# Kernel optimization log

Hardware: AMD Instinct MI355X
Metric: run time of the kernel (lower is better)

The kernel has to match this reference:

```python
import jax, jax.numpy as jnp
import numpy as np

ATOM_DIM = 34
GAT_DIM = 128
HID_DIM = 256
G_LAYERS = 3
ALPHA = 0.2
NEG_INF = -9e15  # matches torch zero_vec constant


def setup_inputs() -> dict:
    key = jax.random.key(0)
    ks = jax.random.split(key, 10)
    B, N = 64, 512
    compound = jax.random.normal(ks[0], (B, N, ATOM_DIM), dtype=jnp.float32)
    adj = jax.random.randint(ks[1], (B, N, N), 0, 2, dtype=jnp.int32)
    # xavier_uniform gain=1.414 approx: bound = gain*sqrt(6/(fan_in+fan_out))
    def xavier(k, shape, gain=1.414):
        bound = gain * np.sqrt(6.0 / (shape[-2] + shape[-1]))
        return jax.random.uniform(k, shape, jnp.float32, -bound, bound)
    W_stack = xavier(ks[2], (G_LAYERS, ATOM_DIM, GAT_DIM))        # per-layer W
    a_stack = xavier(ks[3], (G_LAYERS, 2 * GAT_DIM, 1))            # per-layer a
    W_out = xavier(ks[4], (G_LAYERS * GAT_DIM, GAT_DIM))           # gat_out.W
    a_out = xavier(ks[5], (2 * GAT_DIM, 1))                        # gat_out.a
    lim = 1.0 / np.sqrt(GAT_DIM)
    Wc = jax.random.uniform(ks[6], (GAT_DIM, HID_DIM), jnp.float32, -lim, lim)  # W_comp weight (in,out)
    bc = jax.random.uniform(ks[7], (HID_DIM,), jnp.float32, -lim, lim)
    return {"compound": compound, "adj": adj, "W_stack": W_stack,
            "a_stack": a_stack, "W_out": W_out, "a_out": a_out,
            "Wc": Wc, "bc": bc}


def _gat_layer(h, adj, W, a, concat):
    # h: [B,N,Fin], adj: [B,N,N], W: [Fin,Fout], a: [2*Fout,1]
    Wh = jnp.einsum('bnf,fg->bng', h, W)                 # [B,N,Fout]
    Fout = W.shape[1]
    # e[b,i,j] = leakyrelu(Wh_i . a1 + Wh_j . a2) == leakyrelu(cat(Wh_i,Wh_j) @ a)
    src = Wh @ a[:Fout, 0]                               # [B,N]
    dst = Wh @ a[Fout:, 0]                               # [B,N]
    e = jax.nn.leaky_relu(src[:, :, None] + dst[:, None, :], ALPHA)  # [B,N,N]
    scores = jnp.where(adj > 0, e, NEG_INF)
    attention = jax.nn.softmax(scores, axis=2)
    h_prime = jnp.einsum('bij,bjf->bif', attention, Wh)  # [B,N,Fout]
    return jax.nn.elu(h_prime) if concat else h_prime


def reference(compound, adj, W_stack, a_stack, W_out, a_out, Wc, bc):
    heads = [_gat_layer(compound, adj, W_stack[l], a_stack[l], concat=True)
             for l in range(G_LAYERS)]
    multi = jnp.concatenate(heads, axis=2)               # [B,N,G_LAYERS*GAT_DIM]
    x = jax.nn.elu(_gat_layer(multi, adj, W_out, a_out, concat=False))
    x = jax.nn.leaky_relu(jnp.einsum('bnf,fh->bnh', x, Wc) + bc, ALPHA)
    return x  # [B,N,HID_DIM]
```

## Files before the change

kernel.cpp:

```cpp
#include <hip/hip_runtime.h>
#include <hip/hip_bf16.h>
#include <math.h>


#define ALPHA 0.2f
#define LOG2E 1.44269504088896f

#if __has_builtin(__builtin_amdgcn_exp2f)
#define EXP2F(x) __builtin_amdgcn_exp2f(x)
#else
extern "C" __device__ float __ocml_exp2_f32(float);
#define EXP2F(x) __ocml_exp2_f32(x)
#endif

typedef __attribute__((ext_vector_type(8))) short s16x8;
typedef __attribute__((ext_vector_type(4))) float f32x4;

#define MF(a, b, c) c = __builtin_amdgcn_mfma_f32_16x16x32_bf16(a, b, c, 0, 0, 0)

__device__ __forceinline__ ushort bf16_rne(float f) {
  union { float f; unsigned u; } v; v.f = f;
  unsigned r = v.u + 0x7FFFu + ((v.u >> 16) & 1u);
  return (ushort)(r >> 16);
}
__device__ __forceinline__ float bf16_tof(ushort h) {
  union { unsigned u; float f; } v; v.u = ((unsigned)h) << 16;
  return v.f;
}
__device__ __forceinline__ void split_store4(
    ushort* __restrict__ ph, ushort* __restrict__ pl,
    float v0, float v1, float v2, float v3) {
  ushort h0 = bf16_rne(v0), h1 = bf16_rne(v1), h2 = bf16_rne(v2), h3 = bf16_rne(v3);
  *(ushort4*)ph = make_ushort4(h0, h1, h2, h3);
  *(ushort4*)pl = make_ushort4(bf16_rne(v0 - bf16_tof(h0)), bf16_rne(v1 - bf16_tof(h1)),
                               bf16_rne(v2 - bf16_tof(h2)), bf16_rne(v3 - bf16_tof(h3)));
}

__device__ __forceinline__ long wht_off(long batch, int c, int j) {
  return batch * 65536 + (long)(c >> 4) * 8192 + (j >> 5) * 512 +
         ((c & 15) << 3) + (((j >> 3) & 3) << 7) + (j & 7);
}

__device__ __forceinline__ long w_frag_off(int c, int j, int Kd) {
  return (long)(c >> 4) * (Kd * 16) + (j >> 5) * 512 +
         ((c & 15) << 3) + (((j >> 3) & 3) << 7) + (j & 7);
}

#define WHT_SLOT 8388608L

__global__ __launch_bounds__(256) void front_union(
    const float* __restrict__ A, const float* __restrict__ Wst,
    const float* __restrict__ ast,
    ushort* __restrict__ whtBase, float* __restrict__ srcB, float* __restrict__ dstB,
    const int* __restrict__ adj, unsigned* __restrict__ mask,
    const float* __restrict__ W_out, ushort* __restrict__ WoT_H, ushort* __restrict__ WoT_L)
{
  __shared__ float AsT[34][36];
  __shared__ float Ws[34][128];
  const int t = threadIdx.x;
  const int g = blockIdx.x / 83, r83 = blockIdx.x - g * 83;

  if (r83 >= 48) {
    if (r83 < 80) {
      const int mb = g * 32 + (r83 - 48);
      const int gid = mb * 256 + t;
      const int4* __restrict__ p = (const int4*)(adj + (long)gid * 32);
      unsigned m = 0;
#pragma unroll
      for (int k = 0; k < 8; k++) {
        const int4 v = p[k];
        m |= (v.x > 0 ? 1u : 0u) << (4 * k);
        m |= (v.y > 0 ? 1u : 0u) << (4 * k + 1);
        m |= (v.z > 0 ? 1u : 0u) << (4 * k + 2);
        m |= (v.w > 0 ? 1u : 0u) << (4 * k + 3);
      }
      mask[gid] = m;
    } else {
      const int wb = g * 3 + (r83 - 80);
      const int idx = wb * 256 + t;
      const int k = idx / 128, n = idx % 128;
      const float v = W_out[idx];
      const ushort h = bf16_rne(v);
      const long o = w_frag_off(n, k, 384);
      WoT_H[o] = h;
      WoT_L[o] = bf16_rne(v - bf16_tof(h));
    }
    return;
  }

  const int bid = g * 48 + r83;
  const int l = bid >> 10;
  const float* __restrict__ W = Wst + (long)l * 34 * 128;
  const float* __restrict__ avec = ast + (long)l * 256;
  ushort* __restrict__ whtH = whtBase + (long)l * WHT_SLOT;
  ushort* __restrict__ whtL = whtH + 4194304;
  float* __restrict__ src = srcB + (long)l * 32768;
  float* __restrict__ dst = dstB + (long)l * 32768;
  const long row0 = (long)(bid & 1023) * 32;
  const int cg = t & 31, rg = t >> 5;
  {
    const int r = t >> 3, l8 = t & 7;
#pragma unroll
    for (int q = 0; q < 5; q++) {
      int k = l8 + q * 8;
      if (k < 34) AsT[k][r] = A[(row0 + r) * 34 + k];
    }
  }
  {
    int idx = t;
#pragma unroll
    for (int i = 0; i < 17; i++, idx += 256)
      Ws[idx >> 7][idx & 127] = W[idx];
  }
  __syncthreads();

  float acc[4][4];
#pragma unroll
  for (int r = 0; r < 4; r++)
#pragma unroll
    for (int c = 0; c < 4; c++) acc[r][c] = 0.f;
#pragma unroll 2
  for (int k = 0; k < 34; k++) {
    const float4 wv = *(const float4*)&Ws[k][cg * 4];
    const float4 av = *(const float4*)&AsT[k][rg * 4];
#define GFMA(r, a) \
    acc[r][0] += (a) * wv.x; acc[r][1] += (a) * wv.y; \
    acc[r][2] += (a) * wv.z; acc[r][3] += (a) * wv.w;
    GFMA(0, av.x) GFMA(1, av.y) GFMA(2, av.z) GFMA(3, av.w)
#undef GFMA
  }

  {
    const long batch = row0 >> 9;
    const int j = (int)(row0 & 511) + rg * 4;
#pragma unroll
    for (int cc = 0; cc < 4; cc++) {
      const long o = wht_off(batch, cg * 4 + cc, j);
      split_store4(&whtH[o], &whtL[o], acc[0][cc], acc[1][cc], acc[2][cc], acc[3][cc]);
    }
  }

  const float4 a1 = *(const float4*)&avec[cg * 4];
  const float4 a2 = *(const float4*)&avec[128 + cg * 4];
#pragma unroll
  for (int r = 0; r < 4; r++) {
    float s = acc[r][0]*a1.x + acc[r][1]*a1.y + acc[r][2]*a1.z + acc[r][3]*a1.w;
    float d = acc[r][0]*a2.x + acc[r][1]*a2.y + acc[r][2]*a2.z + acc[r][3]*a2.w;
#pragma unroll
    for (int w = 1; w < 32; w <<= 1) {
      s += __shfl_xor(s, w, 64);
      d += __shfl_xor(d, w, 64);
    }
    if (cg == 0) {
      src[row0 + rg * 4 + r] = s * LOG2E;
      dst[row0 + rg * 4 + r] = d * LOG2E;
    }
  }
}


#define LD_SET(S, KB) \
  S##0H = *(const s16x8*)&bH[(KB) * 512]; \
  S##0L = *(const s16x8*)&bL[(KB) * 512]; \
  S##1H = *(const s16x8*)&bH[8192 + (KB) * 512]; \
  S##1L = *(const s16x8*)&bL[8192 + (KB) * 512];

#define STEP(S, KB) { \
  const int k0_ = ((KB) * 32 + q * 8) ^ ((((KB) >> 1) & 7) << 3); \
  const s16x8 a0_ = *(const s16x8*)&As[m16][k0_]; \
  const s16x8 a1_ = *(const s16x8*)&As[16 + m16][k0_]; \
  MF(a0_, S##0H, acc00); MF(a0_, S##1H, acc01); \
  MF(a1_, S##0H, acc10); MF(a1_, S##1H, acc11); \
  MF(a0_, S##0L, acc00); MF(a0_, S##1L, acc01); \
  MF(a1_, S##0L, acc10); MF(a1_, S##1L, acc11); \
  if ((KB) + 4 < 16) { LD_SET(S, (KB) + 4) } }

__global__ __launch_bounds__(256, 4) void fused_attn(
    const unsigned* __restrict__ mask,
    const float* __restrict__ srcB, const float* __restrict__ dstB,
    const ushort* __restrict__ whtBase,
    float* __restrict__ out, const int ostride)
{
  __shared__ ushort As[32][520];
  __shared__ float dstS[544];
  __shared__ float invS[32];
  __shared__ float wredM[4];
  const int t = threadIdx.x;
  const int l = blockIdx.z;
  const float* __restrict__ src = srcB + (long)l * 32768;
  const float* __restrict__ dstv = dstB + (long)l * 32768;
  const ushort* __restrict__ whtH = whtBase + (long)l * WHT_SLOT;
  const ushort* __restrict__ whtL = whtH + 4194304;
  const int ocoff = l * 128;
  const int flat = blockIdx.y * 16 + blockIdx.x;
  const int swz = (flat & 7) * 128 + (flat >> 3);
  const long base = (long)(swz >> 4) * 512;
  const int i0 = (swz & 15) * 32;

  const int wv = t >> 6, lane = t & 63;
  const int m16 = lane & 15, q = lane >> 4;
  const int n0 = wv * 32;
  const ushort* __restrict__ bH = whtH + base * 128 + wv * 16384 + lane * 8;
  const ushort* __restrict__ bL = whtL + base * 128 + wv * 16384 + lane * 8;
  s16x8 sA0H, sA0L, sA1H, sA1L, sB0H, sB0L, sB1H, sB1L;
  s16x8 sC0H, sC0L, sC1H, sC1L, sD0H, sD0L, sD1H, sD1L;
  LD_SET(sA, 0)
  LD_SET(sB, 1)
  LD_SET(sC, 2)
  LD_SET(sD, 3)
  const int r1 = t >> 3, l8 = t & 7;
  const long irow = base + i0 + r1;
  const float si = src[irow];
  const uint2 mw2 = *(const uint2*)(mask + irow * 16 + 2 * l8);

  {
    const float d0 = dstv[base + t];
    const float d1 = dstv[base + t + 256];
    dstS[t + (t >> 6) * 4] = d0;
    const int t2 = t + 256;
    dstS[t2 + (t2 >> 6) * 4] = d1;
    float mx = fmaxf(d0, d1);
#pragma unroll
    for (int w = 1; w < 64; w <<= 1) mx = fmaxf(mx, __shfl_xor(mx, w, 64));
    if ((t & 63) == 0) wredM[t >> 6] = mx;
  }
  __syncthreads();
  const float md = fmaxf(fmaxf(wredM[0], wredM[1]), fmaxf(wredM[2], wredM[3]));

  {
    const float em = si + md;
    const float m = fmaxf(em, ALPHA * em);
    const float* __restrict__ dp = &dstS[l8 * 68];
    const int jb = l8 * 64;
    const int xs = l8 << 3;
    float sum = 0.f;
#pragma unroll
    for (int g = 0; g < 16; g++) {
      const float4 dv = *(const float4*)&dp[g * 4];
      const unsigned w = ((g & 8) ? mw2.y : mw2.x) >> ((g & 7) * 4);
      float e0 = si + dv.x, e1 = si + dv.y, e2 = si + dv.z, e3 = si + dv.w;
      e0 = fmaxf(e0, ALPHA * e0) - m; e1 = fmaxf(e1, ALPHA * e1) - m;
      e2 = fmaxf(e2, ALPHA * e2) - m; e3 = fmaxf(e3, ALPHA * e3) - m;
      float p0 = EXP2F(e0), p1 = EXP2F(e1), p2 = EXP2F(e2), p3 = EXP2F(e3);
      p0 = (w & 1u) ? p0 : 0.f;
      p1 = (w & 2u) ? p1 : 0.f;
      p2 = (w & 4u) ? p2 : 0.f;
      p3 = (w & 8u) ? p3 : 0.f;
      sum += (p0 + p1) + (p2 + p3);
      union { __hip_bfloat162 b; unsigned u; } u01, u23;
      u01.b = __float22bfloat162_rn(make_float2(p0, p1));
      u23.b = __float22bfloat162_rn(make_float2(p2, p3));
      *(uint2*)&As[r1][(jb + g * 4) ^ xs] = make_uint2(u01.u, u23.u);
    }
#pragma unroll
    for (int w = 1; w < 8; w <<= 1) sum += __shfl_xor(sum, w, 64);
    if (l8 == 0) invS[r1] = 1.f / sum;
  }
  __syncthreads();

  f32x4 acc00 = {0.f,0.f,0.f,0.f}, acc01 = {0.f,0.f,0.f,0.f};
  f32x4 acc10 = {0.f,0.f,0.f,0.f}, acc11 = {0.f,0.f,0.f,0.f};
#pragma unroll
  for (int kp = 0; kp < 4; kp++) {
    STEP(sA, 4 * kp)
    STEP(sB, 4 * kp + 1)
    STEP(sC, 4 * kp + 2)
    STEP(sD, 4 * kp + 3)
  }
#pragma unroll
  for (int reg = 0; reg < 4; reg++) {
    const int row = q * 4 + reg;
    const float li0 = invS[row], li1 = invS[16 + row];
    float v00 = acc00[reg] * li0, v01 = acc01[reg] * li0;
    float v10 = acc10[reg] * li1, v11 = acc11[reg] * li1;
    v00 = v00 > 0.f ? v00 : __expf(v00) - 1.f;
    v01 = v01 > 0.f ? v01 : __expf(v01) - 1.f;
    v10 = v10 > 0.f ? v10 : __expf(v10) - 1.f;
    v11 = v11 > 0.f ? v11 : __expf(v11) - 1.f;
    float* o0 = out + (base + i0 + row) * (long)ostride + ocoff + n0 + m16;
    float* o1 = out + (base + i0 + 16 + row) * (long)ostride + ocoff + n0 + m16;
    o0[0] = v00; o0[16] = v01;
    o1[0] = v10; o1[16] = v11;
  }
}

template<int K, int KC, int MODE>
__global__ __launch_bounds__(256) void mfma_gemm(
    const float* __restrict__ A,
    const ushort* __restrict__ BTH, const ushort* __restrict__ BTL,
    const float* __restrict__ bias, float* __restrict__ outF,
    ushort* __restrict__ whtH, ushort* __restrict__ whtL,
    const float* __restrict__ avec, float* __restrict__ src, float* __restrict__ dst,
    const int ostride)
{
  constexpr int KP = KC + 8;
  __shared__ ushort AsH[32][KP];
  __shared__ ushort AsL[32][KP];
  __shared__ float sredS[4][32], sredD[4][32];
  const int t = threadIdx.x;

  if (MODE == 0 && blockIdx.x >= 1024) {
    const int idx = ((int)blockIdx.x - 1024) * 256 + t;
    const int k = idx >> 8, n = idx & 255;
    const float v = bias[idx];
    const ushort h = bf16_rne(v);
    const long o = w_frag_off(n, k, 128);
    ushort* __restrict__ WcTH = (ushort*)outF;
    WcTH[o] = h;
    WcTH[32768 + o] = bf16_rne(v - bf16_tof(h));
    return;
  }

  const long row0 = (long)blockIdx.x * 32;
  const int ncoff = (MODE == 1) ? blockIdx.y * 128 : 0;

  const int wv = t >> 6, lane = t & 63;
  const int m16 = lane & 15, q = lane >> 4;
  const int n0 = wv * 32;
  const ushort* __restrict__ bh0 = BTH + (long)((ncoff + n0) >> 4) * (K * 16) + lane * 8;
  const ushort* __restrict__ bl0 = BTL + (long)((ncoff + n0) >> 4) * (K * 16) + lane * 8;

  f32x4 acc[2][2];
#pragma unroll
  for (int m = 0; m < 2; m++)
#pragma unroll
    for (int n = 0; n < 2; n++) acc[m][n] = (f32x4){0.f, 0.f, 0.f, 0.f};

  for (int kc = 0; kc < K; kc += KC) {
    constexpr int NIT = (32 * KC / 4) / 256;
#pragma unroll
    for (int it = 0; it < NIT; it++) {
      const int idx = t + it * 256;
      const int r = idx / (KC / 4), k4 = idx % (KC / 4);
      const float4 v = *(const float4*)&A[(row0 + r) * (long)K + kc + k4 * 4];
      split_store4(&AsH[r][k4 * 4], &AsL[r][k4 * 4], v.x, v.y, v.z, v.w);
    }
    __syncthreads();
#pragma unroll
    for (int ks = 0; ks < KC / 32; ks++) {
      const int k0 = ks * 32 + q * 8;
      const s16x8 a0H = *(const s16x8*)&AsH[m16][k0];
      const s16x8 a0L = *(const s16x8*)&AsL[m16][k0];
      const s16x8 a1H = *(const s16x8*)&AsH[16 + m16][k0];
      const s16x8 a1L = *(const s16x8*)&AsL[16 + m16][k0];
      const int bo = ((kc >> 5) + ks) * 512;
      const s16x8 b0H = *(const s16x8*)&bh0[bo];
      const s16x8 b0L = *(const s16x8*)&bl0[bo];
      const s16x8 b1H = *(const s16x8*)&bh0[K * 16 + bo];
      const s16x8 b1L = *(const s16x8*)&bl0[K * 16 + bo];
      acc[0][0] = __builtin_amdgcn_mfma_f32_16x16x32_bf16(a0H, b0H, acc[0][0], 0, 0, 0);
      acc[0][1] = __builtin_amdgcn_mfma_f32_16x16x32_bf16(a0H, b1H, acc[0][1], 0, 0, 0);
      acc[1][0] = __builtin_amdgcn_mfma_f32_16x16x32_bf16(a1H, b0H, acc[1][0], 0, 0, 0);
      acc[1][1] = __builtin_amdgcn_mfma_f32_16x16x32_bf16(a1H, b1H, acc[1][1], 0, 0, 0);
      acc[0][0] = __builtin_amdgcn_mfma_f32_16x16x32_bf16(a0L, b0H, acc[0][0], 0, 0, 0);
      acc[0][1] = __builtin_amdgcn_mfma_f32_16x16x32_bf16(a0L, b1H, acc[0][1], 0, 0, 0);
      acc[1][0] = __builtin_amdgcn_mfma_f32_16x16x32_bf16(a1L, b0H, acc[1][0], 0, 0, 0);
      acc[1][1] = __builtin_amdgcn_mfma_f32_16x16x32_bf16(a1L, b1H, acc[1][1], 0, 0, 0);
      acc[0][0] = __builtin_amdgcn_mfma_f32_16x16x32_bf16(a0H, b0L, acc[0][0], 0, 0, 0);
      acc[0][1] = __builtin_amdgcn_mfma_f32_16x16x32_bf16(a0H, b1L, acc[0][1], 0, 0, 0);
      acc[1][0] = __builtin_amdgcn_mfma_f32_16x16x32_bf16(a1H, b0L, acc[1][0], 0, 0, 0);
      acc[1][1] = __builtin_amdgcn_mfma_f32_16x16x32_bf16(a1H, b1L, acc[1][1], 0, 0, 0);
    }
    __syncthreads();
  }

  if (MODE == 0) {
    const long batch = row0 >> 9;
    const int iloc = (int)(row0 & 511);
#pragma unroll
    for (int m = 0; m < 2; m++)
#pragma unroll
      for (int n = 0; n < 2; n++) {
        const int c = n0 + n * 16 + m16;
        const int j = iloc + m * 16 + q * 4;
        const long o = wht_off(batch, c, j);
        const f32x4 v = acc[m][n];
        split_store4(&whtH[o], &whtL[o], v[0], v[1], v[2], v[3]);
      }
    const float a10 = avec[n0 + m16], a11 = avec[n0 + 16 + m16];
    const float a20 = avec[128 + n0 + m16], a21 = avec[128 + n0 + 16 + m16];
#pragma unroll
    for (int m = 0; m < 2; m++) {
#pragma unroll
      for (int reg = 0; reg < 4; reg++) {
        float s = acc[m][0][reg] * a10 + acc[m][1][reg] * a11;
        float d = acc[m][0][reg] * a20 + acc[m][1][reg] * a21;
#pragma unroll
        for (int w = 1; w < 16; w <<= 1) {
          s += __shfl_xor(s, w, 64);
          d += __shfl_xor(d, w, 64);
        }
        if (m16 == 0) {
          const int row = m * 16 + q * 4 + reg;
          sredS[wv][row] = s;
          sredD[wv][row] = d;
        }
      }
    }
    __syncthreads();
    if (t < 32) {
      const float s = sredS[0][t] + sredS[1][t] + sredS[2][t] + sredS[3][t];
      const float d = sredD[0][t] + sredD[1][t] + sredD[2][t] + sredD[3][t];
      src[row0 + t] = s * LOG2E;
      dst[row0 + t] = d * LOG2E;
    }
  } else {
#pragma unroll
    for (int m = 0; m < 2; m++)
#pragma unroll
      for (int n = 0; n < 2; n++) {
        const int c = ncoff + n0 + n * 16 + m16;
        const float bv = bias[c];
#pragma unroll
        for (int reg = 0; reg < 4; reg++) {
          float v = acc[m][n][reg] + bv;
          v = fmaxf(v, ALPHA * v);
          outF[(row0 + m * 16 + q * 4 + reg) * (long)ostride + c] = v;
        }
      }
  }
}

extern "C" void kernel_launch(void* const* d_in, const int* in_sizes, int n_in,
                              void* d_out, int out_size, void* d_ws, size_t ws_size,
                              hipStream_t stream) {
  const float* compound = (const float*)d_in[0];
  const int*   adj      = (const int*)d_in[1];
  const float* W_stack  = (const float*)d_in[2];
  const float* a_stack  = (const float*)d_in[3];
  const float* W_out    = (const float*)d_in[4];
  const float* a_out    = (const float*)d_in[5];
  const float* Wc       = (const float*)d_in[6];
  const float* bc       = (const float*)d_in[7];
  float* out = (float*)d_out;

  ushort* wht_all = (ushort*)d_ws;
  float* f     = (float*)d_ws;
  float* multi = f + 12582912;
  float* x     = multi;
  ushort* WcT_H = wht_all + WHT_SLOT;
  ushort* WcT_L = WcT_H + 32768;

  unsigned* mask = (unsigned*)d_out;
  float* doutF = (float*)d_out;
  float* srcB = doutF + 524288;
  float* dstB = srcB + 4 * 32768;
  ushort* WoT_H = (ushort*)(dstB + 4 * 32768);
  ushort* WoT_L = WoT_H + 98304;
  float* src3 = srcB + 3 * 32768;
  float* dst3 = dstB + 3 * 32768;

  front_union<<<5312, 256, 0, stream>>>(
      compound, W_stack, a_stack, wht_all, srcB, dstB,
      adj, mask, W_out, WoT_H, WoT_L);
  fused_attn<<<dim3(16, 64, 3), 256, 0, stream>>>(
      mask, srcB, dstB, wht_all, multi, 384);
  mfma_gemm<384, 192, 0><<<1152, 256, 0, stream>>>(
      multi, WoT_H, WoT_L, Wc, (float*)WcT_H, wht_all, wht_all + 4194304,
      a_out, src3, dst3, 0);
  fused_attn<<<dim3(16, 64, 1), 256, 0, stream>>>(
      mask, src3, dst3, wht_all, x, 128);
  mfma_gemm<128, 128, 1><<<dim3(1024, 2), 256, 0, stream>>>(
      x, WcT_H, WcT_L, bc, out, nullptr, nullptr, nullptr, nullptr, nullptr, 256);
}
```

Measured before the change: 223.9 us.

## Fuse final W_comp GEMM with bias and leaky-ReLU into last attention kernel

The last GAT attention kernel now converts its ELU outputs to split bf16 (hi/lo) in shared memory and immediately multiplies them by the pre-packed Wc with MFMA, adding the bias and applying leaky-ReLU before writing the final output. This removes one kernel launch and the round trip of the intermediate x tensor through global memory. Because the output buffer previously also held the mask and src/dst vectors, the mask is copied into workspace by extra blocks of the preceding GEMM kernel, and src3/dst3 move to workspace. The cost is extra MFMA and register work inside the attention kernel, plus a mask copy.

Measured after the change: 221.0 us. No clear change (-1.3%).

```diff
diff --git a/kernel.cpp b/kernel.cpp
--- a/kernel.cpp
+++ b/kernel.cpp
@@ -175,11 +175,13 @@
   MF(a1_, S##0L, acc10); MF(a1_, S##1L, acc11); \
   if ((KB) + 4 < 16) { LD_SET(S, (KB) + 4) } }
 
+template<int FINAL>
 __global__ __launch_bounds__(256, 4) void fused_attn(
     const unsigned* __restrict__ mask,
     const float* __restrict__ srcB, const float* __restrict__ dstB,
     const ushort* __restrict__ whtBase,
-    float* __restrict__ out, const int ostride)
+    float* __restrict__ out, const int ostride,
+    const ushort* __restrict__ wcT, const float* __restrict__ bc)
 {
   __shared__ ushort As[32][520];
   __shared__ float dstS[544];
@@ -267,20 +269,80 @@
     STEP(sC, 4 * kp + 2)
     STEP(sD, 4 * kp + 3)
   }
-#pragma unroll
-  for (int reg = 0; reg < 4; reg++) {
-    const int row = q * 4 + reg;
-    const float li0 = invS[row], li1 = invS[16 + row];
-    float v00 = acc00[reg] * li0, v01 = acc01[reg] * li0;
-    float v10 = acc10[reg] * li1, v11 = acc11[reg] * li1;
-    v00 = v00 > 0.f ? v00 : __expf(v00) - 1.f;
-    v01 = v01 > 0.f ? v01 : __expf(v01) - 1.f;
-    v10 = v10 > 0.f ? v10 : __expf(v10) - 1.f;
-    v11 = v11 > 0.f ? v11 : __expf(v11) - 1.f;
-    float* o0 = out + (base + i0 + row) * (long)ostride + ocoff + n0 + m16;
-    float* o1 = out + (base + i0 + 16 + row) * (long)ostride + ocoff + n0 + m16;
-    o0[0] = v00; o0[16] = v01;
-    o1[0] = v10; o1[16] = v11;
+
+  if (!FINAL) {
+#pragma unroll
+    for (int reg = 0; reg < 4; reg++) {
+      const int row = q * 4 + reg;
+      const float li0 = invS[row], li1 = invS[16 + row];
+      float v00 = acc00[reg] * li0, v01 = acc01[reg] * li0;
+      float v10 = acc10[reg] * li1, v11 = acc11[reg] * li1;
+      v00 = v00 > 0.f ? v00 : __expf(v00) - 1.f;
+      v01 = v01 > 0.f ? v01 : __expf(v01) - 1.f;
+      v10 = v10 > 0.f ? v10 : __expf(v10) - 1.f;
+      v11 = v11 > 0.f ? v11 : __expf(v11) - 1.f;
+      float* o0 = out + (base + i0 + row) * (long)ostride + ocoff + n0 + m16;
+      float* o1 = out + (base + i0 + 16 + row) * (long)ostride + ocoff + n0 + m16;
+      o0[0] = v00; o0[16] = v01;
+      o1[0] = v10; o1[16] = v11;
+    }
+  } else {
+    __syncthreads();
+#pragma unroll
+    for (int reg = 0; reg < 4; reg++) {
+      const int row = q * 4 + reg;
+      const float li0 = invS[row], li1 = invS[16 + row];
+      float v00 = acc00[reg] * li0, v01 = acc01[reg] * li0;
+      float v10 = acc10[reg] * li1, v11 = acc11[reg] * li1;
+      v00 = v00 > 0.f ? v00 : __expf(v00) - 1.f;
+      v01 = v01 > 0.f ? v01 : __expf(v01) - 1.f;
+      v10 = v10 > 0.f ? v10 : __expf(v10) - 1.f;
+      v11 = v11 > 0.f ? v11 : __expf(v11) - 1.f;
+      ushort h;
+      h = bf16_rne(v00); As[row][n0 + m16] = h;
+      As[row][264 + n0 + m16] = bf16_rne(v00 - bf16_tof(h));
+      h = bf16_rne(v01); As[row][n0 + 16 + m16] = h;
+      As[row][264 + n0 + 16 + m16] = bf16_rne(v01 - bf16_tof(h));
+      h = bf16_rne(v10); As[16 + row][n0 + m16] = h;
+      As[16 + row][264 + n0 + m16] = bf16_rne(v10 - bf16_tof(h));
+      h = bf16_rne(v11); As[16 + row][n0 + 16 + m16] = h;
+      As[16 + row][264 + n0 + 16 + m16] = bf16_rne(v11 - bf16_tof(h));
+    }
+    __syncthreads();
+    f32x4 a2[2][4];
+#pragma unroll
+    for (int m2 = 0; m2 < 2; m2++)
+#pragma unroll
+      for (int n = 0; n < 4; n++) a2[m2][n] = (f32x4){0.f, 0.f, 0.f, 0.f};
+#pragma unroll
+    for (int kb = 0; kb < 4; kb++) {
+      const int k0 = kb * 32 + q * 8;
+      const s16x8 aH0 = *(const s16x8*)&As[m16][k0];
+      const s16x8 aL0 = *(const s16x8*)&As[m16][264 + k0];
+      const s16x8 aH1 = *(const s16x8*)&As[16 + m16][k0];
+      const s16x8 aL1 = *(const s16x8*)&As[16 + m16][264 + k0];
+#pragma unroll
+      for (int n = 0; n < 4; n++) {
+        const ushort* wp = wcT + (wv * 4 + n) * 2048 + kb * 512 + lane * 8;
+        const s16x8 bh = *(const s16x8*)wp;
+        const s16x8 bl = *(const s16x8*)(wp + 32768);
+        MF(aH0, bh, a2[0][n]); MF(aL0, bh, a2[0][n]); MF(aH0, bl, a2[0][n]);
+        MF(aH1, bh, a2[1][n]); MF(aL1, bh, a2[1][n]); MF(aH1, bl, a2[1][n]);
+      }
+    }
+#pragma unroll
+    for (int m2 = 0; m2 < 2; m2++)
+#pragma unroll
+      for (int n = 0; n < 4; n++) {
+        const int c = wv * 64 + n * 16 + m16;
+        const float bv = bc[c];
+#pragma unroll
+        for (int reg = 0; reg < 4; reg++) {
+          float v = a2[m2][n][reg] + bv;
+          v = fmaxf(v, ALPHA * v);
+          out[(base + i0 + m2 * 16 + q * 4 + reg) * 256L + c] = v;
+        }
+      }
   }
 }
 
@@ -291,7 +353,8 @@
     const float* __restrict__ bias, float* __restrict__ outF,
     ushort* __restrict__ whtH, ushort* __restrict__ whtL,
     const float* __restrict__ avec, float* __restrict__ src, float* __restrict__ dst,
-    const int ostride)
+    const int ostride,
+    const unsigned* __restrict__ maskSrc, unsigned* __restrict__ maskDst)
 {
   constexpr int KP = KC + 8;
   __shared__ ushort AsH[32][KP];
@@ -300,14 +363,25 @@
   const int t = threadIdx.x;
 
   if (MODE == 0 && blockIdx.x >= 1024) {
-    const int idx = ((int)blockIdx.x - 1024) * 256 + t;
-    const int k = idx >> 8, n = idx & 255;
-    const float v = bias[idx];
-    const ushort h = bf16_rne(v);
-    const long o = w_frag_off(n, k, 128);
-    ushort* __restrict__ WcTH = (ushort*)outF;
-    WcTH[o] = h;
-    WcTH[32768 + o] = bf16_rne(v - bf16_tof(h));
+    const int xb = (int)blockIdx.x - 1024;
+    if (xb < 128) {
+      const int idx = xb * 256 + t;
+      const int k = idx >> 8, n = idx & 255;
+      const float v = bias[idx];
+      const ushort h = bf16_rne(v);
+      const long o = w_frag_off(n, k, 128);
+      ushort* __restrict__ WcTH = (ushort*)outF;
+      WcTH[o] = h;
+      WcTH[32768 + o] = bf16_rne(v - bf16_tof(h));
+    } else {
+      const int gid = (xb - 128) * 256 + t;
+      const uint4* __restrict__ s4 = (const uint4*)maskSrc;
+      uint4* __restrict__ d4 = (uint4*)maskDst;
+      d4[gid] = s4[gid];
+      d4[gid + 32768] = s4[gid + 32768];
+      d4[gid + 65536] = s4[gid + 65536];
+      d4[gid + 98304] = s4[gid + 98304];
+    }
     return;
   }
 
@@ -437,9 +511,10 @@
   ushort* wht_all = (ushort*)d_ws;
   float* f     = (float*)d_ws;
   float* multi = f + 12582912;
-  float* x     = multi;
   ushort* WcT_H = wht_all + WHT_SLOT;
-  ushort* WcT_L = WcT_H + 32768;
+  unsigned* maskS1 = (unsigned*)(wht_all + WHT_SLOT + 65536);
+  float* src3b = (float*)(wht_all + WHT_SLOT + 65536 + 1048576);
+  float* dst3b = src3b + 32768;
 
   unsigned* mask = (unsigned*)d_out;
   float* doutF = (float*)d_out;
@@ -447,19 +522,15 @@
   float* dstB = srcB + 4 * 32768;
   ushort* WoT_H = (ushort*)(dstB + 4 * 32768);
   ushort* WoT_L = WoT_H + 98304;
-  float* src3 = srcB + 3 * 32768;
-  float* dst3 = dstB + 3 * 32768;
 
   front_union<<<5312, 256, 0, stream>>>(
       compound, W_stack, a_stack, wht_all, srcB, dstB,
       adj, mask, W_out, WoT_H, WoT_L);
-  fused_attn<<<dim3(16, 64, 3), 256, 0, stream>>>(
-      mask, srcB, dstB, wht_all, multi, 384);
-  mfma_gemm<384, 192, 0><<<1152, 256, 0, stream>>>(
+  fused_attn<0><<<dim3(16, 64, 3), 256, 0, stream>>>(
+      mask, srcB, dstB, wht_all, multi, 384, nullptr, nullptr);
+  mfma_gemm<384, 192, 0><<<1280, 256, 0, stream>>>(
       multi, WoT_H, WoT_L, Wc, (float*)WcT_H, wht_all, wht_all + 4194304,
-      a_out, src3, dst3, 0);
-  fused_attn<<<dim3(16, 64, 1), 256, 0, stream>>>(
-      mask, src3, dst3, wht_all, x, 128);
-  mfma_gemm<128, 128, 1><<<dim3(1024, 2), 256, 0, stream>>>(
-      x, WcT_H, WcT_L, bc, out, nullptr, nullptr, nullptr, nullptr, nullptr, 256);
-}
+      a_out, src3b, dst3b, 0, mask, maskS1);
+  fused_attn<1><<<dim3(16, 64, 1), 256, 0, stream>>>(
+      maskS1, src3b, dst3b, wht_all, out, 256, WcT_H, bc);
+}
```
